# Performance work log

Measured on AMD Instinct MI355X. Metric: run time of the kernel, lower is better.

The kernel has to match this reference:

```python
import jax, jax.numpy as jnp
import numpy as np

K_RATIO = 0.2
EPS = 1e-6


def setup_inputs() -> dict:
    key = jax.random.key(0)
    k1, k2 = jax.random.split(key)
    B, C, D, H, W = 2, 4, 128, 128, 128
    logits = jax.random.normal(k1, (B, C, D, H, W), dtype=jnp.float32)
    labels = jax.random.randint(k2, (B, D, H, W), 0, C)
    # one-hot target along channel axis 1, matching the tensor-path `target` arg
    target = jax.nn.one_hot(labels, C, axis=1, dtype=jnp.float32)
    return {"logits": logits, "target": target}


def reference(logits, target):
    B, C = logits.shape[0], logits.shape[1]

    # ---- Top-K cross entropy (ignore_index=-1 -> all voxels valid) ----
    y = jnp.argmax(target, axis=1)  # [B, D, H, W] int labels
    logp = jax.nn.log_softmax(logits, axis=1)
    # CE per voxel: -logp[b, y, d, h, w]
    ce = -jnp.take_along_axis(logp, y[:, None], axis=1)[:, 0]  # [B, D, H, W]
    ce_flat = ce.reshape(B, -1)  # [B, N]
    N = ce_flat.shape[1]
    k = max(1, int(N * K_RATIO))  # static: all voxels valid, k < N
    topk_vals, _ = jax.lax.top_k(ce_flat, k)  # [B, k]
    topk_loss = jnp.mean(jnp.mean(topk_vals, axis=1))

    # ---- Soft dice (no valid_mask in tensor path) ----
    p = jax.nn.softmax(logits, axis=1)  # [B, C, D, H, W]
    spatial = tuple(range(2, p.ndim))
    num = 2.0 * jnp.sum(p * target, axis=spatial)          # [B, C]
    den = jnp.sum(p + target, axis=spatial) + EPS          # [B, C]
    dice = 1.0 - num / den                                  # [B, C]
    if C > 1:
        dice = dice[:, 1:]  # drop background channel
    dice_loss = jnp.mean(dice)

    return topk_loss + 0.5 * dice_loss
```

## Files before the change

kernel.cpp:

```cpp
#include <hip/hip_runtime.h>
#include <stdint.h>

#define NVOX (1u << 21)
#define NB   2
#define KSEL 419430u
#define TPB  256
#define VPB  4096
#define BPB  ((int)(NVOX / VPB))
#define NBLK (NB * BPB)
#define NCOPY 64
#define NHC  16
#define NBINS 4096
#define SH   19
#define FIXS 262144.0f

__device__ __forceinline__ float wred64(float v) {
#pragma unroll
  for (int o = 32; o > 0; o >>= 1) v += __shfl_down(v, o, 64);
  return v;
}

__global__ __launch_bounds__(TPB, 4) void k1_fused(
    const float* __restrict__ logits, const float* __restrict__ target,
    uint32_t* __restrict__ hcnt, float* __restrict__ hsum,
    float* __restrict__ dice_acc )
{
  __shared__ unsigned long long hbin[NBINS];
  const int tid = threadIdx.x;
  for (int i = tid; i < NBINS; i += TPB) hbin[i] = 0ull;
  __syncthreads();

  const int blk = blockIdx.x;
  const int b = blk / BPB;
  const size_t v0 = (size_t)(blk % BPB) * VPB;
  const float* lg = logits + (size_t)b * 4 * NVOX + v0;
  const float* tg = target + (size_t)b * 4 * NVOX + v0;

  float sp[4] = {0.f,0.f,0.f,0.f}, nm[4] = {0.f,0.f,0.f,0.f}, ct[4] = {0.f,0.f,0.f,0.f};

  for (int i = tid * 4; i < VPB; i += TPB * 4) {
    float4 L[4], T[4];
#pragma unroll
    for (int c = 0; c < 4; ++c) {
      L[c] = *(const float4*)(lg + (size_t)c * NVOX + i);
      T[c] = *(const float4*)(tg + (size_t)c * NVOX + i);
    }
#pragma unroll
    for (int j = 0; j < 4; ++j) {
      float l[4], t[4];
#pragma unroll
      for (int c = 0; c < 4; ++c) {
        l[c] = ((const float*)&L[c])[j];
        t[c] = ((const float*)&T[c])[j];
      }
      float m = fmaxf(fmaxf(l[0], l[1]), fmaxf(l[2], l[3]));
      float e[4]; float s = 0.f;
#pragma unroll
      for (int c = 0; c < 4; ++c) { e[c] = __expf(l[c] - m); s += e[c]; }
      float inv = 1.f / s;
      float lse = __logf(s);
      float ly = l[0]*t[0] + l[1]*t[1] + l[2]*t[2] + l[3]*t[3];
      float cev = (m - ly) + lse;
      uint32_t idx = __float_as_uint(cev) >> SH;
      if (idx > NBINS - 1) idx = NBINS - 1;
      unsigned long long pk = (1ull << 40) | (unsigned long long)(cev * FIXS);
      atomicAdd(&hbin[idx], pk);
#pragma unroll
      for (int c = 0; c < 4; ++c) {
        float p = e[c] * inv;
        sp[c] += p;
        nm[c] += p * t[c];
        ct[c] += t[c];
      }
    }
  }

#pragma unroll
  for (int c = 0; c < 4; ++c) { sp[c] = wred64(sp[c]); nm[c] = wred64(nm[c]); ct[c] = wred64(ct[c]); }
  if ((tid & 63) == 0) {
    float* dst = dice_acc + ((size_t)(blk & (NCOPY - 1)) * NB + b) * 12;
#pragma unroll
    for (int c = 0; c < 4; ++c) {
      atomicAdd(dst + c,     sp[c]);
      atomicAdd(dst + 4 + c, nm[c]);
      atomicAdd(dst + 8 + c, ct[c]);
    }
  }
  __syncthreads();
  const size_t hoff = ((size_t)b * NHC + (size_t)(blk & (NHC - 1))) * NBINS;
  uint32_t* cdst = hcnt + hoff;
  float*    sdst = hsum + hoff;
  for (int i = tid; i < NBINS; i += TPB) {
    unsigned long long v = hbin[i];
    if (v) {
      atomicAdd(&cdst[i], (uint32_t)(v >> 40));
      atomicAdd(&sdst[i], (float)(v & 0xFFFFFFFFFFull) * (1.0f / FIXS));
    }
  }
}

__global__ __launch_bounds__(256) void k_reduce(
    const uint32_t* __restrict__ hcnt, const float* __restrict__ hsum,
    uint32_t* __restrict__ rcnt, float* __restrict__ rsum)
{
  const int b = blockIdx.x >> 2;
  const int seg = blockIdx.x & 3;
  const int base = seg * 1024 + threadIdx.x * 4;
  uint4 c = {0,0,0,0};
  float4 s = {0.f,0.f,0.f,0.f};
  for (int copy = 0; copy < NHC; ++copy) {
    const size_t off = ((size_t)b * NHC + copy) * NBINS + base;
    uint4 cv = *(const uint4*)(hcnt + off);
    float4 sv = *(const float4*)(hsum + off);
    c.x += cv.x; c.y += cv.y; c.z += cv.z; c.w += cv.w;
    s.x += sv.x; s.y += sv.y; s.z += sv.z; s.w += sv.w;
  }
  *(uint4*)(rcnt + (size_t)b * NBINS + base) = c;
  *(float4*)(rsum + (size_t)b * NBINS + base) = s;
}

__global__ __launch_bounds__(256) void k_final(
    const uint32_t* __restrict__ rcnt, const float* __restrict__ rsum,
    const float* __restrict__ dice_acc, float* __restrict__ out)
{
  __shared__ uint32_t shc[NBINS];
  __shared__ uint32_t chunk[256];
  __shared__ uint32_t sbkt, srem;
  __shared__ float wpart[4];
  __shared__ float ts[NB];
  __shared__ float comp[24];
  const int tid = threadIdx.x;

  for (int b = 0; b < NB; ++b) {
    const uint32_t* rc = rcnt + (size_t)b * NBINS;
    const float*    rs = rsum + (size_t)b * NBINS;
    uint32_t s = 0;
#pragma unroll
    for (int q = 0; q < 4; ++q) {
      uint4 v = *(const uint4*)(rc + tid * 16 + q * 4);
      *(uint4*)&shc[tid * 16 + q * 4] = v;
      s += v.x + v.y + v.z + v.w;
    }
    chunk[tid] = s;
    __syncthreads();
    if (tid == 0) {
      uint32_t k = KSEL, cum = 0;
      int ci = 255;
      for (; ci > 0; --ci) {
        uint32_t c = chunk[ci];
        if (cum + c >= k) break;
        cum += c;
      }
      int bkt = ci * 16;
      for (int j = 15; j >= 0; --j) {
        uint32_t c = shc[ci * 16 + j];
        if (cum + c >= k) { bkt = ci * 16 + j; break; }
        cum += c;
      }
      sbkt = (uint32_t)bkt;
      srem = k - cum;
    }
    __syncthreads();
    const int bkt = (int)sbkt;
    float w = 0.f;
#pragma unroll
    for (int j = 0; j < 16; ++j) {
      int bin = tid * 16 + j;
      if (bin > bkt) w += rs[bin];
    }
    w = wred64(w);
    if ((tid & 63) == 0) wpart[tid >> 6] = w;
    __syncthreads();
    if (tid == 0) {
      float cnt_t = (float)shc[bkt];
      float sum_t = rs[bkt];
      float lo = __uint_as_float((uint32_t)bkt << SH);
      float hi = __uint_as_float((uint32_t)(bkt + 1) << SH);
      float width = hi - lo;
      float avg = sum_t / cnt_t;
      float frac = (float)srem / cnt_t;
      float est = avg + (1.f - frac) * 0.5f * width;
      ts[b] = wpart[0] + wpart[1] + wpart[2] + wpart[3] + (float)srem * est;
    }
    __syncthreads();
  }

  if (tid < 24) {
    float a = 0.f;
    for (int r = 0; r < NCOPY; ++r) a += dice_acc[(size_t)r * 24 + tid];
    comp[tid] = a;
  }
  __syncthreads();
  if (tid == 0) {
    float dl = 0.f;
#pragma unroll
    for (int b = 0; b < 2; ++b)
#pragma unroll
      for (int c = 1; c < 4; ++c) {
        float sp = comp[b * 12 + c];
        float nm = comp[b * 12 + 4 + c];
        float ct = comp[b * 12 + 8 + c];
        dl += 1.f - (2.f * nm) / (sp + ct + 1e-6f);
      }
    float topk = 0.5f * (ts[0] + ts[1]) / (float)KSEL;
    out[0] = topk + 0.5f * (dl / 6.f);
  }
}

extern "C" void kernel_launch(void* const* d_in, const int* in_sizes, int n_in,
                              void* d_out, int out_size, void* d_ws, size_t ws_size,
                              hipStream_t stream) {
  (void)in_sizes; (void)n_in; (void)out_size; (void)ws_size;
  const float* logits = (const float*)d_in[0];
  const float* target = (const float*)d_in[1];
  float* out = (float*)d_out;

  char* ws = (char*)d_ws;
  uint32_t* hcnt = (uint32_t*)ws;
  float*    hsum = (float*)(hcnt + (size_t)NB * NHC * NBINS);
  float*    dice_acc = hsum + (size_t)NB * NHC * NBINS;
  uint32_t* rcnt = (uint32_t*)(dice_acc + (size_t)NCOPY * NB * 12);
  float*    rsum = (float*)(rcnt + (size_t)NB * NBINS);
  const size_t ZERO_BYTES = (size_t)((char*)(dice_acc + (size_t)NCOPY * NB * 12) - ws);

  hipMemsetAsync(hcnt, 0, ZERO_BYTES, stream);

  k1_fused<<<NBLK, TPB, 0, stream>>>(logits, target, hcnt, hsum, dice_acc);
  k_reduce<<<NB * 4, 256, 0, stream>>>(hcnt, hsum, rcnt, rsum);
  k_final<<<1, 256, 0, stream>>>(rcnt, rsum, dice_acc, out);
}
```

Baseline: 176.3 us.

## Write CE to workspace, use count-only histogram, sum above threshold in second pass

The main kernel now keeps only 32-bit counts in a shared histogram instead of packed 64-bit count+fixed-point sums, and writes per-voxel CE values to workspace. A new pick kernel merges the histogram copies and finds the threshold bucket. A sum kernel then rereads the CE array to sum the values above and inside that bucket. Block size drops to 2048 voxels with higher occupancy bounds. This trades cheaper shared atomics for an extra 16MB write and read of CE values plus an extra launch.

```diff
diff --git a/kernel.cpp b/kernel.cpp
--- a/kernel.cpp
+++ b/kernel.cpp
@@ -5,14 +5,16 @@
 #define NB   2
 #define KSEL 419430u
 #define TPB  256
-#define VPB  4096
+#define VPB  2048
 #define BPB  ((int)(NVOX / VPB))
 #define NBLK (NB * BPB)
 #define NCOPY 64
 #define NHC  16
 #define NBINS 4096
 #define SH   19
-#define FIXS 262144.0f
+#define SVPB 4096
+#define SBPB ((int)(NVOX / SVPB))
+#define SBLK (NB * SBPB)
 
 __device__ __forceinline__ float wred64(float v) {
 #pragma unroll
@@ -20,14 +22,14 @@
   return v;
 }
 
-__global__ __launch_bounds__(TPB, 4) void k1_fused(
+__global__ __launch_bounds__(TPB, 8) void k1_fused(
     const float* __restrict__ logits, const float* __restrict__ target,
-    uint32_t* __restrict__ hcnt, float* __restrict__ hsum,
+    float* __restrict__ ce, uint32_t* __restrict__ hcnt,
     float* __restrict__ dice_acc )
 {
-  __shared__ unsigned long long hbin[NBINS];
+  __shared__ uint32_t hbin[NBINS];
   const int tid = threadIdx.x;
-  for (int i = tid; i < NBINS; i += TPB) hbin[i] = 0ull;
+  for (int i = tid; i < NBINS; i += TPB) hbin[i] = 0u;
   __syncthreads();
 
   const int blk = blockIdx.x;
@@ -35,16 +37,20 @@
   const size_t v0 = (size_t)(blk % BPB) * VPB;
   const float* lg = logits + (size_t)b * 4 * NVOX + v0;
   const float* tg = target + (size_t)b * 4 * NVOX + v0;
+  float* cd = ce + (size_t)b * NVOX + v0;
 
   float sp[4] = {0.f,0.f,0.f,0.f}, nm[4] = {0.f,0.f,0.f,0.f}, ct[4] = {0.f,0.f,0.f,0.f};
 
-  for (int i = tid * 4; i < VPB; i += TPB * 4) {
+#pragma unroll
+  for (int it = 0; it < VPB / (TPB * 4); ++it) {
+    const int i = it * (TPB * 4) + tid * 4;
     float4 L[4], T[4];
 #pragma unroll
     for (int c = 0; c < 4; ++c) {
       L[c] = *(const float4*)(lg + (size_t)c * NVOX + i);
       T[c] = *(const float4*)(tg + (size_t)c * NVOX + i);
     }
+    float4 cv;
 #pragma unroll
     for (int j = 0; j < 4; ++j) {
       float l[4], t[4];
@@ -61,10 +67,10 @@
       float lse = __logf(s);
       float ly = l[0]*t[0] + l[1]*t[1] + l[2]*t[2] + l[3]*t[3];
       float cev = (m - ly) + lse;
+      ((float*)&cv)[j] = cev;
       uint32_t idx = __float_as_uint(cev) >> SH;
       if (idx > NBINS - 1) idx = NBINS - 1;
-      unsigned long long pk = (1ull << 40) | (unsigned long long)(cev * FIXS);
-      atomicAdd(&hbin[idx], pk);
+      atomicAdd(&hbin[idx], 1u);
 #pragma unroll
       for (int c = 0; c < 4; ++c) {
         float p = e[c] * inv;
@@ -73,6 +79,7 @@
         ct[c] += t[c];
       }
     }
+    *(float4*)(cd + i) = cv;
   }
 
 #pragma unroll
@@ -89,109 +96,118 @@
   __syncthreads();
   const size_t hoff = ((size_t)b * NHC + (size_t)(blk & (NHC - 1))) * NBINS;
   uint32_t* cdst = hcnt + hoff;
-  float*    sdst = hsum + hoff;
   for (int i = tid; i < NBINS; i += TPB) {
-    unsigned long long v = hbin[i];
-    if (v) {
-      atomicAdd(&cdst[i], (uint32_t)(v >> 40));
-      atomicAdd(&sdst[i], (float)(v & 0xFFFFFFFFFFull) * (1.0f / FIXS));
-    }
-  }
-}
-
-__global__ __launch_bounds__(256) void k_reduce(
-    const uint32_t* __restrict__ hcnt, const float* __restrict__ hsum,
-    uint32_t* __restrict__ rcnt, float* __restrict__ rsum)
-{
-  const int b = blockIdx.x >> 2;
-  const int seg = blockIdx.x & 3;
-  const int base = seg * 1024 + threadIdx.x * 4;
-  uint4 c = {0,0,0,0};
-  float4 s = {0.f,0.f,0.f,0.f};
-  for (int copy = 0; copy < NHC; ++copy) {
-    const size_t off = ((size_t)b * NHC + copy) * NBINS + base;
-    uint4 cv = *(const uint4*)(hcnt + off);
-    float4 sv = *(const float4*)(hsum + off);
-    c.x += cv.x; c.y += cv.y; c.z += cv.z; c.w += cv.w;
-    s.x += sv.x; s.y += sv.y; s.z += sv.z; s.w += sv.w;
-  }
-  *(uint4*)(rcnt + (size_t)b * NBINS + base) = c;
-  *(float4*)(rsum + (size_t)b * NBINS + base) = s;
-}
-
-__global__ __launch_bounds__(256) void k_final(
-    const uint32_t* __restrict__ rcnt, const float* __restrict__ rsum,
-    const float* __restrict__ dice_acc, float* __restrict__ out)
+    uint32_t v = hbin[i];
+    if (v) atomicAdd(&cdst[i], v);
+  }
+}
+
+__global__ __launch_bounds__(256) void k_pick(
+    const uint32_t* __restrict__ hcnt, uint32_t* __restrict__ pick)
 {
   __shared__ uint32_t shc[NBINS];
   __shared__ uint32_t chunk[256];
-  __shared__ uint32_t sbkt, srem;
-  __shared__ float wpart[4];
-  __shared__ float ts[NB];
+  const int b = blockIdx.x;
+  const int tid = threadIdx.x;
+  uint32_t acc[16];
+#pragma unroll
+  for (int q = 0; q < 16; ++q) acc[q] = 0u;
+  for (int copy = 0; copy < NHC; ++copy) {
+    const uint32_t* src = hcnt + ((size_t)b * NHC + copy) * NBINS + tid * 16;
+#pragma unroll
+    for (int q = 0; q < 4; ++q) {
+      uint4 v = *(const uint4*)(src + q * 4);
+      acc[q*4+0] += v.x; acc[q*4+1] += v.y; acc[q*4+2] += v.z; acc[q*4+3] += v.w;
+    }
+  }
+  uint32_t s = 0;
+#pragma unroll
+  for (int q = 0; q < 16; ++q) { shc[tid * 16 + q] = acc[q]; s += acc[q]; }
+  chunk[tid] = s;
+  __syncthreads();
+  if (tid == 0) {
+    uint32_t k = KSEL, cum = 0;
+    int ci = 255;
+    for (; ci > 0; --ci) {
+      uint32_t c = chunk[ci];
+      if (cum + c >= k) break;
+      cum += c;
+    }
+    int bkt = ci * 16;
+    for (int j = 15; j >= 0; --j) {
+      uint32_t c = shc[ci * 16 + j];
+      if (cum + c >= k) { bkt = ci * 16 + j; break; }
+      cum += c;
+    }
+    pick[b * 4 + 0] = (uint32_t)bkt;
+    pick[b * 4 + 1] = k - cum;
+    pick[b * 4 + 2] = shc[bkt];
+  }
+}
+
+__global__ __launch_bounds__(256) void k_sum(
+    const float* __restrict__ ce, const uint32_t* __restrict__ pick,
+    float* __restrict__ tacc )
+{
+  const int blk = blockIdx.x;
+  const int b = blk / SBPB;
+  const uint32_t bkt = pick[b * 4];
+  const float4* src = (const float4*)(ce + (size_t)b * NVOX + (size_t)(blk % SBPB) * SVPB);
+  float4 v[4];
+#pragma unroll
+  for (int q = 0; q < 4; ++q) v[q] = src[threadIdx.x + q * 256];
+  float ab = 0.f, ti = 0.f;
+#pragma unroll
+  for (int q = 0; q < 4; ++q) {
+#pragma unroll
+    for (int j = 0; j < 4; ++j) {
+      float x = ((const float*)&v[q])[j];
+      uint32_t idx = __float_as_uint(x) >> SH;
+      if (idx > NBINS - 1) idx = NBINS - 1;
+      ab += (idx > bkt)  ? x : 0.f;
+      ti += (idx == bkt) ? x : 0.f;
+    }
+  }
+  ab = wred64(ab); ti = wred64(ti);
+  if ((threadIdx.x & 63) == 0) {
+    float* d = tacc + ((size_t)(blk & (NCOPY - 1)) * NB + b) * 2;
+    atomicAdd(d,     ab);
+    atomicAdd(d + 1, ti);
+  }
+}
+
+__global__ __launch_bounds__(256) void k_final(
+    const uint32_t* __restrict__ pick, const float* __restrict__ tacc,
+    const float* __restrict__ dice_acc, float* __restrict__ out)
+{
   __shared__ float comp[24];
+  __shared__ float tt[4];
   const int tid = threadIdx.x;
-
-  for (int b = 0; b < NB; ++b) {
-    const uint32_t* rc = rcnt + (size_t)b * NBINS;
-    const float*    rs = rsum + (size_t)b * NBINS;
-    uint32_t s = 0;
-#pragma unroll
-    for (int q = 0; q < 4; ++q) {
-      uint4 v = *(const uint4*)(rc + tid * 16 + q * 4);
-      *(uint4*)&shc[tid * 16 + q * 4] = v;
-      s += v.x + v.y + v.z + v.w;
-    }
-    chunk[tid] = s;
-    __syncthreads();
-    if (tid == 0) {
-      uint32_t k = KSEL, cum = 0;
-      int ci = 255;
-      for (; ci > 0; --ci) {
-        uint32_t c = chunk[ci];
-        if (cum + c >= k) break;
-        cum += c;
-      }
-      int bkt = ci * 16;
-      for (int j = 15; j >= 0; --j) {
-        uint32_t c = shc[ci * 16 + j];
-        if (cum + c >= k) { bkt = ci * 16 + j; break; }
-        cum += c;
-      }
-      sbkt = (uint32_t)bkt;
-      srem = k - cum;
-    }
-    __syncthreads();
-    const int bkt = (int)sbkt;
-    float w = 0.f;
-#pragma unroll
-    for (int j = 0; j < 16; ++j) {
-      int bin = tid * 16 + j;
-      if (bin > bkt) w += rs[bin];
-    }
-    w = wred64(w);
-    if ((tid & 63) == 0) wpart[tid >> 6] = w;
-    __syncthreads();
-    if (tid == 0) {
-      float cnt_t = (float)shc[bkt];
-      float sum_t = rs[bkt];
-      float lo = __uint_as_float((uint32_t)bkt << SH);
-      float hi = __uint_as_float((uint32_t)(bkt + 1) << SH);
-      float width = hi - lo;
-      float avg = sum_t / cnt_t;
-      float frac = (float)srem / cnt_t;
-      float est = avg + (1.f - frac) * 0.5f * width;
-      ts[b] = wpart[0] + wpart[1] + wpart[2] + wpart[3] + (float)srem * est;
-    }
-    __syncthreads();
-  }
-
   if (tid < 24) {
     float a = 0.f;
     for (int r = 0; r < NCOPY; ++r) a += dice_acc[(size_t)r * 24 + tid];
     comp[tid] = a;
+  } else if (tid >= 32 && tid < 36) {
+    const int j = tid - 32;
+    float a = 0.f;
+    for (int r = 0; r < NCOPY; ++r) a += tacc[(size_t)r * 4 + j];
+    tt[j] = a;
   }
   __syncthreads();
   if (tid == 0) {
+    float ts2 = 0.f;
+#pragma unroll
+    for (int b = 0; b < NB; ++b) {
+      uint32_t bkt = pick[b * 4], rem = pick[b * 4 + 1], cnt = pick[b * 4 + 2];
+      float above = tt[b * 2], ties = tt[b * 2 + 1];
+      float lo = __uint_as_float(bkt << SH);
+      float hi = __uint_as_float((bkt + 1) << SH);
+      float width = hi - lo;
+      float avg = ties / (float)cnt;
+      float frac = (float)rem / (float)cnt;
+      float est = avg + (1.f - frac) * 0.5f * width;
+      ts2 += above + (float)rem * est;
+    }
     float dl = 0.f;
 #pragma unroll
     for (int b = 0; b < 2; ++b)
@@ -202,7 +218,7 @@
         float ct = comp[b * 12 + 8 + c];
         dl += 1.f - (2.f * nm) / (sp + ct + 1e-6f);
       }
-    float topk = 0.5f * (ts[0] + ts[1]) / (float)KSEL;
+    float topk = 0.5f * ts2 / (float)KSEL;
     out[0] = topk + 0.5f * (dl / 6.f);
   }
 }
@@ -217,15 +233,16 @@
 
   char* ws = (char*)d_ws;
   uint32_t* hcnt = (uint32_t*)ws;
-  float*    hsum = (float*)(hcnt + (size_t)NB * NHC * NBINS);
-  float*    dice_acc = hsum + (size_t)NB * NHC * NBINS;
-  uint32_t* rcnt = (uint32_t*)(dice_acc + (size_t)NCOPY * NB * 12);
-  float*    rsum = (float*)(rcnt + (size_t)NB * NBINS);
-  const size_t ZERO_BYTES = (size_t)((char*)(dice_acc + (size_t)NCOPY * NB * 12) - ws);
-
-  hipMemsetAsync(hcnt, 0, ZERO_BYTES, stream);
-
-  k1_fused<<<NBLK, TPB, 0, stream>>>(logits, target, hcnt, hsum, dice_acc);
-  k_reduce<<<NB * 4, 256, 0, stream>>>(hcnt, hsum, rcnt, rsum);
-  k_final<<<1, 256, 0, stream>>>(rcnt, rsum, dice_acc, out);
-}
+  float*    dice_acc = (float*)(ws + (size_t)NB * NHC * NBINS * 4);
+  float*    tacc = dice_acc + (size_t)NCOPY * NB * 12;
+  uint32_t* pick = (uint32_t*)(tacc + (size_t)NCOPY * NB * 2);
+  float*    ce = (float*)((char*)pick + 32);
+  const size_t ZERO_BYTES = (size_t)((char*)pick - ws);
+
+  hipMemsetAsync(ws, 0, ZERO_BYTES, stream);
+
+  k1_fused<<<NBLK, TPB, 0, stream>>>(logits, target, ce, hcnt, dice_acc);
+  k_pick<<<NB, 256, 0, stream>>>(hcnt, pick);
+  k_sum<<<SBLK, 256, 0, stream>>>(ce, pick, tacc);
+  k_final<<<1, 256, 0, stream>>>(pick, tacc, dice_acc, out);
+}
```

New measurement: 206.7 us. +17.2%, slower.

## Flush packed 64-bit histogram atomics and software-prefetch next tile

Applied to the files above, without the earlier changes.

The per-block shared histogram is flushed to global memory as single packed 64-bit integer atomics instead of separate 32-bit count and float sum atomics. This halves the global atomic count and makes the bucket sums exact fixed-point. The reduce kernel unpacks the counts and sums. The main loop double-buffers the float4 loads so the next tile's logits and targets are fetched while the current one is computed. The final kernel sums the dice partials with shared atomics across all threads, and the added register buffers may increase register pressure.

```diff
diff --git a/kernel.cpp b/kernel.cpp
--- a/kernel.cpp
+++ b/kernel.cpp
@@ -8,12 +8,15 @@
 #define VPB  4096
 #define BPB  ((int)(NVOX / VPB))
 #define NBLK (NB * BPB)
+#define NITER ((int)(VPB / (TPB * 4)))
 #define NCOPY 64
 #define NHC  16
 #define NBINS 4096
 #define SH   19
 #define FIXS 262144.0f
 
+typedef unsigned long long ull;
+
 __device__ __forceinline__ float wred64(float v) {
 #pragma unroll
   for (int o = 32; o > 0; o >>= 1) v += __shfl_down(v, o, 64);
@@ -22,10 +25,10 @@
 
 __global__ __launch_bounds__(TPB, 4) void k1_fused(
     const float* __restrict__ logits, const float* __restrict__ target,
-    uint32_t* __restrict__ hcnt, float* __restrict__ hsum,
+    ull* __restrict__ hist,
     float* __restrict__ dice_acc )
 {
-  __shared__ unsigned long long hbin[NBINS];
+  __shared__ ull hbin[NBINS];
   const int tid = threadIdx.x;
   for (int i = tid; i < NBINS; i += TPB) hbin[i] = 0ull;
   __syncthreads();
@@ -38,20 +41,30 @@
 
   float sp[4] = {0.f,0.f,0.f,0.f}, nm[4] = {0.f,0.f,0.f,0.f}, ct[4] = {0.f,0.f,0.f,0.f};
 
-  for (int i = tid * 4; i < VPB; i += TPB * 4) {
-    float4 L[4], T[4];
-#pragma unroll
-    for (int c = 0; c < 4; ++c) {
-      L[c] = *(const float4*)(lg + (size_t)c * NVOX + i);
-      T[c] = *(const float4*)(tg + (size_t)c * NVOX + i);
+  float4 La[4], Ta[4], Lb[4], Tb[4];
+#pragma unroll
+  for (int c = 0; c < 4; ++c) {
+    La[c] = *(const float4*)(lg + (size_t)c * NVOX + tid * 4);
+    Ta[c] = *(const float4*)(tg + (size_t)c * NVOX + tid * 4);
+  }
+
+#pragma unroll
+  for (int it = 0; it < NITER; ++it) {
+    if (it + 1 < NITER) {
+      const int inx = (it + 1) * (TPB * 4) + tid * 4;
+#pragma unroll
+      for (int c = 0; c < 4; ++c) {
+        Lb[c] = *(const float4*)(lg + (size_t)c * NVOX + inx);
+        Tb[c] = *(const float4*)(tg + (size_t)c * NVOX + inx);
+      }
     }
 #pragma unroll
     for (int j = 0; j < 4; ++j) {
       float l[4], t[4];
 #pragma unroll
       for (int c = 0; c < 4; ++c) {
-        l[c] = ((const float*)&L[c])[j];
-        t[c] = ((const float*)&T[c])[j];
+        l[c] = ((const float*)&La[c])[j];
+        t[c] = ((const float*)&Ta[c])[j];
       }
       float m = fmaxf(fmaxf(l[0], l[1]), fmaxf(l[2], l[3]));
       float e[4]; float s = 0.f;
@@ -63,7 +76,7 @@
       float cev = (m - ly) + lse;
       uint32_t idx = __float_as_uint(cev) >> SH;
       if (idx > NBINS - 1) idx = NBINS - 1;
-      unsigned long long pk = (1ull << 40) | (unsigned long long)(cev * FIXS);
+      ull pk = (1ull << 40) | (ull)(cev * FIXS);
       atomicAdd(&hbin[idx], pk);
 #pragma unroll
       for (int c = 0; c < 4; ++c) {
@@ -73,6 +86,10 @@
         ct[c] += t[c];
       }
     }
+    if (it + 1 < NITER) {
+#pragma unroll
+      for (int c = 0; c < 4; ++c) { La[c] = Lb[c]; Ta[c] = Tb[c]; }
+    }
   }
 
 #pragma unroll
@@ -88,35 +105,31 @@
   }
   __syncthreads();
   const size_t hoff = ((size_t)b * NHC + (size_t)(blk & (NHC - 1))) * NBINS;
-  uint32_t* cdst = hcnt + hoff;
-  float*    sdst = hsum + hoff;
+  ull* hdst = hist + hoff;
   for (int i = tid; i < NBINS; i += TPB) {
-    unsigned long long v = hbin[i];
-    if (v) {
-      atomicAdd(&cdst[i], (uint32_t)(v >> 40));
-      atomicAdd(&sdst[i], (float)(v & 0xFFFFFFFFFFull) * (1.0f / FIXS));
-    }
+    ull v = hbin[i];
+    if (v) atomicAdd(&hdst[i], v);
   }
 }
 
 __global__ __launch_bounds__(256) void k_reduce(
-    const uint32_t* __restrict__ hcnt, const float* __restrict__ hsum,
+    const ull* __restrict__ hist,
     uint32_t* __restrict__ rcnt, float* __restrict__ rsum)
 {
-  const int b = blockIdx.x >> 2;
-  const int seg = blockIdx.x & 3;
-  const int base = seg * 1024 + threadIdx.x * 4;
-  uint4 c = {0,0,0,0};
-  float4 s = {0.f,0.f,0.f,0.f};
+  const int b = blockIdx.x >> 3;
+  const int base = (blockIdx.x & 7) * 512 + threadIdx.x * 2;
+  uint32_t c0 = 0, c1 = 0;
+  ull s0 = 0, s1 = 0;
   for (int copy = 0; copy < NHC; ++copy) {
-    const size_t off = ((size_t)b * NHC + copy) * NBINS + base;
-    uint4 cv = *(const uint4*)(hcnt + off);
-    float4 sv = *(const float4*)(hsum + off);
-    c.x += cv.x; c.y += cv.y; c.z += cv.z; c.w += cv.w;
-    s.x += sv.x; s.y += sv.y; s.z += sv.z; s.w += sv.w;
-  }
-  *(uint4*)(rcnt + (size_t)b * NBINS + base) = c;
-  *(float4*)(rsum + (size_t)b * NBINS + base) = s;
+    const ull* src = hist + ((size_t)b * NHC + copy) * NBINS + base;
+    ull v0 = src[0], v1 = src[1];
+    c0 += (uint32_t)(v0 >> 40); s0 += (v0 & 0xFFFFFFFFFFull);
+    c1 += (uint32_t)(v1 >> 40); s1 += (v1 & 0xFFFFFFFFFFull);
+  }
+  rcnt[(size_t)b * NBINS + base]     = c0;
+  rcnt[(size_t)b * NBINS + base + 1] = c1;
+  rsum[(size_t)b * NBINS + base]     = (float)((double)s0 * (1.0 / 262144.0));
+  rsum[(size_t)b * NBINS + base + 1] = (float)((double)s1 * (1.0 / 262144.0));
 }
 
 __global__ __launch_bounds__(256) void k_final(
@@ -130,6 +143,7 @@
   __shared__ float ts[NB];
   __shared__ float comp[24];
   const int tid = threadIdx.x;
+  if (tid < 24) comp[tid] = 0.f;
 
   for (int b = 0; b < NB; ++b) {
     const uint32_t* rc = rcnt + (size_t)b * NBINS;
@@ -185,11 +199,8 @@
     __syncthreads();
   }
 
-  if (tid < 24) {
-    float a = 0.f;
-    for (int r = 0; r < NCOPY; ++r) a += dice_acc[(size_t)r * 24 + tid];
-    comp[tid] = a;
-  }
+  for (int x = tid; x < NCOPY * 24; x += 256)
+    atomicAdd(&comp[x % 24], dice_acc[x]);
   __syncthreads();
   if (tid == 0) {
     float dl = 0.f;
@@ -216,16 +227,15 @@
   float* out = (float*)d_out;
 
   char* ws = (char*)d_ws;
-  uint32_t* hcnt = (uint32_t*)ws;
-  float*    hsum = (float*)(hcnt + (size_t)NB * NHC * NBINS);
-  float*    dice_acc = hsum + (size_t)NB * NHC * NBINS;
+  ull*      hist = (ull*)ws;
+  float*    dice_acc = (float*)(hist + (size_t)NB * NHC * NBINS);
   uint32_t* rcnt = (uint32_t*)(dice_acc + (size_t)NCOPY * NB * 12);
   float*    rsum = (float*)(rcnt + (size_t)NB * NBINS);
-  const size_t ZERO_BYTES = (size_t)((char*)(dice_acc + (size_t)NCOPY * NB * 12) - ws);
-
-  hipMemsetAsync(hcnt, 0, ZERO_BYTES, stream);
-
-  k1_fused<<<NBLK, TPB, 0, stream>>>(logits, target, hcnt, hsum, dice_acc);
-  k_reduce<<<NB * 4, 256, 0, stream>>>(hcnt, hsum, rcnt, rsum);
+  const size_t ZERO_BYTES = (size_t)((char*)rcnt - ws);
+
+  hipMemsetAsync(ws, 0, ZERO_BYTES, stream);
+
+  k1_fused<<<NBLK, TPB, 0, stream>>>(logits, target, hist, dice_acc);
+  k_reduce<<<NB * 8, 256, 0, stream>>>(hist, rcnt, rsum);
   k_final<<<1, 256, 0, stream>>>(rcnt, rsum, dice_acc, out);
 }
```

Result: no change. 175.1 us (-0.7%).
